# Kernel tuning notes

Hardware: AMD Instinct MI355X
Metric: run time of the kernel (lower is better)

Reference implementation:

```python
import jax, jax.numpy as jnp
import numpy as np

N_NODES = 50000
N_EDGES = 1000000
N_HID = 64
N_GRAPHS = 500
IN_DIM = 4


def setup_inputs() -> dict:
    key = jax.random.key(0)
    ks = jax.random.split(key, 10)
    x = jax.random.normal(ks[0], (N_NODES, IN_DIM), dtype=jnp.float32)
    edge_index = jax.random.randint(ks[1], (2, N_EDGES), 0, N_NODES, dtype=jnp.int64)
    batch = jnp.sort(jax.random.randint(ks[2], (N_NODES,), 0, N_GRAPHS, dtype=jnp.int64))
    # learned parameters (glorot-ish init)
    W1 = jax.random.normal(ks[3], (IN_DIM, N_HID), dtype=jnp.float32) / np.sqrt(IN_DIM)
    b1 = jnp.zeros((N_HID,), dtype=jnp.float32)
    W2 = jax.random.normal(ks[4], (N_HID, N_HID), dtype=jnp.float32) / np.sqrt(N_HID)
    b2 = jnp.zeros((N_HID,), dtype=jnp.float32)
    W3 = jax.random.normal(ks[5], (N_HID, 1), dtype=jnp.float32) / np.sqrt(N_HID)
    b3 = jnp.zeros((1,), dtype=jnp.float32)
    return {"x": x, "edge_index": edge_index, "batch": batch,
            "W1": W1, "b1": b1, "W2": W2, "b2": b2, "W3": W3, "b3": b3}


def gcn_conv(x, W, b, src, dst, num_nodes):
    """PyG GCNConv: x@W, add self-loops, sym deg^-1/2 norm, scatter-add aggregate, +bias."""
    h = x @ W  # [N, D]
    loop = jnp.arange(num_nodes, dtype=src.dtype)
    s = jnp.concatenate([src, loop])  # source nodes (messages gathered from)
    d = jnp.concatenate([dst, loop])  # target nodes (messages scattered to)
    deg = jax.ops.segment_sum(jnp.ones_like(d, dtype=h.dtype), d, num_segments=num_nodes)
    dis = jnp.where(deg > 0, jax.lax.rsqrt(jnp.maximum(deg, 1e-12)), 0.0)
    norm = dis[s] * dis[d]  # [E+N]
    msg = h[s] * norm[:, None]  # gather + scale: the memory-bound hot loop
    out = jax.ops.segment_sum(msg, d, num_segments=num_nodes)
    return out + b


def reference(x, edge_index, batch, W1, b1, W2, b2, W3, b3):
    src, dst = edge_index[0], edge_index[1]
    n = x.shape[0]
    h = gcn_conv(x, W1, b1, src, dst, n)
    h = jax.nn.elu(h)
    # F.dropout with training=False (eval mode) is identity
    h = gcn_conv(h, W2, b2, src, dst, n)
    h = jax.nn.elu(h)
    # scatter-mean pooling over graphs
    sums = jax.ops.segment_sum(h, batch, num_segments=N_GRAPHS)
    cnts = jax.ops.segment_sum(jnp.ones((n,), dtype=h.dtype), batch, num_segments=N_GRAPHS)
    pooled = sums / jnp.maximum(cnts, 1.0)[:, None]
    return pooled @ W3 + b3  # [N_GRAPHS, 1]
```

## Files before the change

kernel.cpp:

```cpp
#include <hip/hip_runtime.h>
#include <hip/hip_fp16.h>
#include <math.h>

#define N_NODES 50000
#define N_EDGES 1000000
#define N_HID 64
#define N_GRAPHS 500
#define IN_DIM 4
#define NPAD 50048

#define BK_SHIFT 7
#define BK_NODES 128
#define NBUCK 391
#define BCAP 3072
#define EPT 16
#define EPW (EPT * 256)
#define NWG_BIN ((N_EDGES + EPW - 1) / EPW)

__global__ void k_init(int* bcur, int* gstart, int* gend, float* sums) {
    int i = blockIdx.x * blockDim.x + threadIdx.x;
    if (i < 512) { bcur[i] = 0; gstart[i] = 0; gend[i] = 0; }
    if (i < N_GRAPHS * N_HID) sums[i] = 0.f;
}

__global__ void k_bin(const int* __restrict__ ei, int* bcur, int* __restrict__ P) {
    __shared__ int hist[NBUCK];
    __shared__ int base[NBUCK];
    int t = threadIdx.x;
    int wg0 = blockIdx.x * EPW;
    for (int b = t; b < NBUCK; b += 256) hist[b] = 0;
    __syncthreads();

    const int4* s4 = (const int4*)ei;
    const int4* d4 = (const int4*)(ei + N_EDGES);
    int rs[EPT], rd[EPT], rl[EPT];
#pragma unroll
    for (int i = 0; i < 4; ++i) {
        int e = wg0 + (i * 256 + t) * 4;
        if (e < N_EDGES) {
            int4 vs = s4[e >> 2];
            int4 vd = d4[e >> 2];
            rs[i * 4 + 0] = vs.x; rd[i * 4 + 0] = vd.x;
            rs[i * 4 + 1] = vs.y; rd[i * 4 + 1] = vd.y;
            rs[i * 4 + 2] = vs.z; rd[i * 4 + 2] = vd.z;
            rs[i * 4 + 3] = vs.w; rd[i * 4 + 3] = vd.w;
            rl[i * 4 + 0] = atomicAdd(&hist[vd.x >> BK_SHIFT], 1);
            rl[i * 4 + 1] = atomicAdd(&hist[vd.y >> BK_SHIFT], 1);
            rl[i * 4 + 2] = atomicAdd(&hist[vd.z >> BK_SHIFT], 1);
            rl[i * 4 + 3] = atomicAdd(&hist[vd.w >> BK_SHIFT], 1);
        } else {
            rd[i * 4 + 0] = rd[i * 4 + 1] = rd[i * 4 + 2] = rd[i * 4 + 3] = -1;
        }
    }
    __syncthreads();
    for (int b = t; b < NBUCK; b += 256) {
        int h = hist[b];
        base[b] = h ? atomicAdd(&bcur[b], h) : 0;
    }
    __syncthreads();
#pragma unroll
    for (int i = 0; i < EPT; ++i) {
        if (rd[i] >= 0) {
            int bk = rd[i] >> BK_SHIFT;
            int loc = base[bk] + rl[i];
            if (loc > BCAP - 1) loc = BCAP - 1;
            P[(size_t)bk * BCAP + loc] = (rs[i] << BK_SHIFT) | (rd[i] & (BK_NODES - 1));
        }
    }
}

__global__ void k_build(const int* __restrict__ bcur, const int* __restrict__ P,
                        const float* __restrict__ x,
                        int* __restrict__ srcidx, int* __restrict__ offs,
                        int* __restrict__ endp, float* __restrict__ dis,
                        float* __restrict__ xs) {
    __shared__ int sp[BCAP];
    __shared__ int scnt[BK_NODES];
    __shared__ int sscan[BK_NODES];
    __shared__ int scur[BK_NODES];
    int b = blockIdx.x;
    int t = threadIdx.x;
    int n = bcur[b];
    if (n > BCAP) n = BCAP;
    if (t < BK_NODES) scnt[t] = 0;
    __syncthreads();
    for (int i = t; i < n; i += 256) {
        int v = P[(size_t)b * BCAP + i];
        sp[i] = v;
        atomicAdd(&scnt[v & (BK_NODES - 1)], 1);
    }
    __syncthreads();
    if (t < BK_NODES) sscan[t] = scnt[t];
    __syncthreads();
    for (int d = 1; d < BK_NODES; d <<= 1) {
        int v = 0;
        if (t < BK_NODES && t >= d) v = sscan[t - d];
        __syncthreads();
        if (t < BK_NODES) sscan[t] += v;
        __syncthreads();
    }
    if (t < BK_NODES) {
        int excl = sscan[t] - scnt[t];
        scur[t] = excl;
        int node = b * BK_NODES + t;
        if (node < N_NODES) {
            int o = b * BCAP + excl;
            offs[node] = o;
            endp[node] = o + scnt[t];
            float dd = 1.0f / sqrtf((float)(scnt[t] + 1));
            dis[node] = dd;
            float4 xv = ((const float4*)x)[node];
            xv.x *= dd; xv.y *= dd; xv.z *= dd; xv.w *= dd;
            ((float4*)xs)[node] = xv;
        }
    }
    __syncthreads();
    for (int i = t; i < n; i += 256) {
        int v = sp[i];
        int ln = v & (BK_NODES - 1);
        int pos = b * BCAP + atomicAdd(&scur[ln], 1);
        srcidx[pos] = v >> BK_SHIFT;
    }
}

__global__ void k_layer1(const float* __restrict__ xs, const int* __restrict__ offs,
                         const int* __restrict__ endp, const int* __restrict__ srcidx,
                         const float* __restrict__ dis, const int* __restrict__ batch,
                         const float* __restrict__ W1, const float* __restrict__ b1,
                         int* __restrict__ gstart, int* __restrict__ gend,
                         __half* __restrict__ h1s) {
    __shared__ float4 sagg[256];
    __shared__ float sdis[256];
    __shared__ float sW1[IN_DIM * N_HID];
    __shared__ float sb1[N_HID];
    int t = threadIdx.x;
    int nb = blockIdx.x * 256;
    int i = nb + t;
    sW1[t] = W1[t];
    if (t < N_HID) sb1[t] = b1[t];
    if (i < N_NODES) {
        int g = batch[i];
        if (i == 0 || batch[i - 1] != g) gstart[g] = i;
        if (i == N_NODES - 1 || batch[i + 1] != g) gend[g] = i + 1;
        const float4* xs4 = (const float4*)xs;
        float4 a0 = xs4[i];
        float4 a1 = make_float4(0.f, 0.f, 0.f, 0.f);
        float4 a2 = a1, a3 = a1;
        int q = offs[i], e = endp[i];
        for (; q + 4 <= e; q += 4) {
            int i0 = srcidx[q], i1 = srcidx[q + 1], i2 = srcidx[q + 2], i3 = srcidx[q + 3];
            float4 v0 = xs4[i0], v1 = xs4[i1], v2 = xs4[i2], v3 = xs4[i3];
            a0.x += v0.x; a0.y += v0.y; a0.z += v0.z; a0.w += v0.w;
            a1.x += v1.x; a1.y += v1.y; a1.z += v1.z; a1.w += v1.w;
            a2.x += v2.x; a2.y += v2.y; a2.z += v2.z; a2.w += v2.w;
            a3.x += v3.x; a3.y += v3.y; a3.z += v3.z; a3.w += v3.w;
        }
        for (; q < e; ++q) {
            float4 v = xs4[srcidx[q]];
            a0.x += v.x; a0.y += v.y; a0.z += v.z; a0.w += v.w;
        }
        float dd = dis[i];
        float4 r;
        r.x = (a0.x + a1.x + a2.x + a3.x) * dd;
        r.y = (a0.y + a1.y + a2.y + a3.y) * dd;
        r.z = (a0.z + a1.z + a2.z + a3.z) * dd;
        r.w = (a0.w + a1.w + a2.w + a3.w) * dd;
        sagg[t] = r;
        sdis[t] = dd;
    } else {
        sagg[t] = make_float4(0.f, 0.f, 0.f, 0.f);
        sdis[t] = 0.f;
    }
    __syncthreads();
    int w = t >> 6, j = t & 63;
    float w0 = sW1[0 * N_HID + j], w1 = sW1[1 * N_HID + j];
    float w2 = sW1[2 * N_HID + j], w3 = sW1[3 * N_HID + j];
    float bj = sb1[j];
    for (int n = 0; n < 64; ++n) {
        int local = w * 64 + n;
        int node = nb + local;
        if (node >= N_NODES) break;
        float4 a = sagg[local];
        float acc = a.x * w0 + a.y * w1 + a.z * w2 + a.w * w3 + bj;
        acc = acc > 0.f ? acc : expm1f(acc);
        h1s[(size_t)node * N_HID + j] = __float2half_rn(acc * sdis[local]);
    }
}

__device__ inline void acc_half8(float* acc, float4 raw) {
    const __half2* hp = (const __half2*)&raw;
#pragma unroll
    for (int c = 0; c < 4; ++c) {
        float2 f = __half22float2(hp[c]);
        acc[2 * c + 0] += f.x;
        acc[2 * c + 1] += f.y;
    }
}

#define L2_NODES 16
__global__ void k_layer2(const __half* __restrict__ h1s, const int* __restrict__ offs,
                         const int* __restrict__ endp, const int* __restrict__ srcidx,
                         const float* __restrict__ dis, const int* __restrict__ batch,
                         const float* __restrict__ W2, const float* __restrict__ b2,
                         float* __restrict__ sums) {
    __shared__ float sAT[N_HID][L2_NODES + 1];
    __shared__ int sbat[L2_NODES];
    int t = threadIdx.x;
    int nb = blockIdx.x * L2_NODES;
    if (t < L2_NODES) sbat[t] = batch[nb + t];

    int wv = t >> 6, lane = t & 63;
    int g = lane >> 3, l = lane & 7;
    const float4* hsv = (const float4*)h1s;
    for (int nn = 0; nn < 4; ++nn) {
        int local = wv * 4 + nn;
        int node = nb + local;
        int start = offs[node], end = endp[node];
        float accA[8] = {0.f, 0.f, 0.f, 0.f, 0.f, 0.f, 0.f, 0.f};
        float accB[8] = {0.f, 0.f, 0.f, 0.f, 0.f, 0.f, 0.f, 0.f};
        if (g == 0) acc_half8(accA, hsv[(size_t)node * 8 + l]);
        for (int base = start; base < end; base += 64) {
            int nc = end - base; if (nc > 64) nc = 64;
            int myidx = (base + lane < end) ? srcidx[base + lane] : 0;
            int q = 0;
            for (; q + 16 <= nc; q += 16) {
                int s0 = __shfl(myidx, q + g);
                int s1 = __shfl(myidx, q + 8 + g);
                float4 r0 = hsv[(size_t)s0 * 8 + l];
                float4 r1 = hsv[(size_t)s1 * 8 + l];
                acc_half8(accA, r0);
                acc_half8(accB, r1);
            }
            if (q + 8 <= nc) {
                int s = __shfl(myidx, q + g);
                acc_half8(accA, hsv[(size_t)s * 8 + l]);
                q += 8;
            }
            {
                int s = __shfl(myidx, q + g);
                if (q + g < nc) acc_half8(accB, hsv[(size_t)s * 8 + l]);
            }
        }
#pragma unroll
        for (int c = 0; c < 8; ++c) accA[c] += accB[c];
#pragma unroll
        for (int c = 0; c < 8; ++c) {
            accA[c] += __shfl_xor(accA[c], 8);
            accA[c] += __shfl_xor(accA[c], 16);
            accA[c] += __shfl_xor(accA[c], 32);
        }
        if (g == 0) {
            float dw = dis[node];
#pragma unroll
            for (int c = 0; c < 8; ++c) sAT[8 * l + c][local] = accA[c] * dw;
        }
    }
    __syncthreads();

    int tj = t & 15, tn = t >> 4;
    const float4* W2v = (const float4*)W2;
    float4 acc = make_float4(0.f, 0.f, 0.f, 0.f);
#pragma unroll 8
    for (int k = 0; k < N_HID; ++k) {
        float a = sAT[k][tn];
        float4 w = W2v[k * 16 + tj];
        acc.x += a * w.x; acc.y += a * w.y; acc.z += a * w.z; acc.w += a * w.w;
    }
    float4 bb = ((const float4*)b2)[tj];
    __syncthreads();
    {
        float4 r;
        r.x = acc.x + bb.x; r.y = acc.y + bb.y;
        r.z = acc.z + bb.z; r.w = acc.w + bb.w;
        r.x = r.x > 0.f ? r.x : expm1f(r.x);
        r.y = r.y > 0.f ? r.y : expm1f(r.y);
        r.z = r.z > 0.f ? r.z : expm1f(r.z);
        r.w = r.w > 0.f ? r.w : expm1f(r.w);
        sAT[4 * tj + 0][tn] = r.x;
        sAT[4 * tj + 1][tn] = r.y;
        sAT[4 * tj + 2][tn] = r.z;
        sAT[4 * tj + 3][tn] = r.w;
    }
    __syncthreads();

    if (t < 64) {
        int s = 0;
        while (s < L2_NODES) {
            int gg = sbat[s];
            int e = s + 1;
            while (e < L2_NODES && sbat[e] == gg) ++e;
            float p = 0.f;
            for (int n = s; n < e; ++n) p += sAT[t][n];
            atomicAdd(&sums[gg * N_HID + t], p);
            s = e;
        }
    }
}

__global__ void k_final(const float* __restrict__ sums, const int* __restrict__ gstart,
                        const int* __restrict__ gend, const float* __restrict__ W3,
                        const float* __restrict__ b3, float* __restrict__ out) {
    int gid = blockIdx.x * 4 + (threadIdx.x >> 6);
    int j = threadIdx.x & 63;
    if (gid >= N_GRAPHS) return;
    int cnt = gend[gid] - gstart[gid];
    float v = sums[gid * N_HID + j] / (float)(cnt > 0 ? cnt : 1);
    float p = v * W3[j];
#pragma unroll
    for (int off = 32; off; off >>= 1) p += __shfl_down(p, off);
    if (j == 0) out[gid] = p + b3[0];
}

extern "C" void kernel_launch(void* const* d_in, const int* in_sizes, int n_in,
                              void* d_out, int out_size, void* d_ws, size_t ws_size,
                              hipStream_t stream) {
    const float* x   = (const float*)d_in[0];
    const int*   ei  = (const int*)d_in[1];
    const int*   bat = (const int*)d_in[2];
    const float* W1  = (const float*)d_in[3];
    const float* b1  = (const float*)d_in[4];
    const float* W2  = (const float*)d_in[5];
    const float* b2  = (const float*)d_in[6];
    const float* W3  = (const float*)d_in[7];
    const float* b3  = (const float*)d_in[8];
    float* out = (float*)d_out;

    char* w = (char*)d_ws;
    int*   bcur   = (int*)w;   w += 512 * 4;
    int*   offs   = (int*)w;   w += NPAD * 4;
    int*   endp   = (int*)w;   w += NPAD * 4;
    float* dis    = (float*)w; w += NPAD * 4;
    int*   gstart = (int*)w;   w += 512 * 4;
    int*   gend   = (int*)w;   w += 512 * 4;
    float* sums   = (float*)w; w += (size_t)N_GRAPHS * N_HID * 4;
    float* xs     = (float*)w; w += (size_t)NPAD * IN_DIM * 4;
    int*   srcidx = (int*)w;   w += (size_t)NBUCK * BCAP * 4;
    int*   P      = (int*)w;   w += (size_t)NBUCK * BCAP * 4;
    __half* h1s   = (__half*)w; w += (size_t)N_NODES * N_HID * 2;

    const int B = 256;
    const int gN = (N_NODES + B - 1) / B;

    k_init<<<(N_GRAPHS * N_HID + B - 1) / B, B, 0, stream>>>(bcur, gstart, gend, sums);
    k_bin<<<NWG_BIN, B, 0, stream>>>(ei, bcur, P);
    k_build<<<NBUCK, B, 0, stream>>>(bcur, P, x, srcidx, offs, endp, dis, xs);

    k_layer1<<<gN, B, 0, stream>>>(xs, offs, endp, srcidx, dis, bat, W1, b1,
                                   gstart, gend, h1s);

    k_layer2<<<N_NODES / L2_NODES, B, 0, stream>>>(
        h1s, offs, endp, srcidx, dis, bat, W2, b2, sums);

    k_final<<<(N_GRAPHS + 3) / 4, B, 0, stream>>>(sums, gstart, gend, W3, b3, out);
}
```

Baseline: 99.60 us.

## Split layer-1 features into two half planes and gather each in separate passes

Layer 1 now writes its fp16 output as two 32-column planes instead of one 64-column row per node. Layer 2 makes two passes, each gathering only one plane, so the working set each pass touches is half the size and fits the cache better. It also prefetches the next node's offsets and source indices before reducing the current node. The cost is that the edge index lists are read twice, each gather moves 8 bytes instead of 16, and the number of gather instructions doubles.

```diff
diff --git a/kernel.cpp b/kernel.cpp
--- a/kernel.cpp
+++ b/kernel.cpp
@@ -128,7 +128,7 @@
                          const float* __restrict__ dis, const int* __restrict__ batch,
                          const float* __restrict__ W1, const float* __restrict__ b1,
                          int* __restrict__ gstart, int* __restrict__ gend,
-                         __half* __restrict__ h1s) {
+                         __half* __restrict__ h1a, __half* __restrict__ h1b) {
     __shared__ float4 sagg[256];
     __shared__ float sdis[256];
     __shared__ float sW1[IN_DIM * N_HID];
@@ -183,26 +183,25 @@
         float4 a = sagg[local];
         float acc = a.x * w0 + a.y * w1 + a.z * w2 + a.w * w3 + bj;
         acc = acc > 0.f ? acc : expm1f(acc);
-        h1s[(size_t)node * N_HID + j] = __float2half_rn(acc * sdis[local]);
-    }
-}
-
-__device__ inline void acc_half8(float* acc, float4 raw) {
+        __half hv = __float2half_rn(acc * sdis[local]);
+        if (j < 32) h1a[(size_t)node * 32 + j] = hv;
+        else        h1b[(size_t)node * 32 + (j - 32)] = hv;
+    }
+}
+
+__device__ inline void acc_half4(float* acc, float2 raw) {
     const __half2* hp = (const __half2*)&raw;
-#pragma unroll
-    for (int c = 0; c < 4; ++c) {
-        float2 f = __half22float2(hp[c]);
-        acc[2 * c + 0] += f.x;
-        acc[2 * c + 1] += f.y;
-    }
+    float2 f0 = __half22float2(hp[0]);
+    float2 f1 = __half22float2(hp[1]);
+    acc[0] += f0.x; acc[1] += f0.y; acc[2] += f1.x; acc[3] += f1.y;
 }
 
 #define L2_NODES 16
-__global__ void k_layer2(const __half* __restrict__ h1s, const int* __restrict__ offs,
-                         const int* __restrict__ endp, const int* __restrict__ srcidx,
-                         const float* __restrict__ dis, const int* __restrict__ batch,
-                         const float* __restrict__ W2, const float* __restrict__ b2,
-                         float* __restrict__ sums) {
+__global__ void k_layer2(const __half* __restrict__ h1a, const __half* __restrict__ h1b,
+                         const int* __restrict__ offs, const int* __restrict__ endp,
+                         const int* __restrict__ srcidx, const float* __restrict__ dis,
+                         const int* __restrict__ batch, const float* __restrict__ W2,
+                         const float* __restrict__ b2, float* __restrict__ sums) {
     __shared__ float sAT[N_HID][L2_NODES + 1];
     __shared__ int sbat[L2_NODES];
     int t = threadIdx.x;
@@ -211,48 +210,63 @@
 
     int wv = t >> 6, lane = t & 63;
     int g = lane >> 3, l = lane & 7;
-    const float4* hsv = (const float4*)h1s;
-    for (int nn = 0; nn < 4; ++nn) {
-        int local = wv * 4 + nn;
-        int node = nb + local;
+#pragma unroll
+    for (int p = 0; p < 2; ++p) {
+        const float2* hv = (const float2*)(p == 0 ? h1a : h1b);
+        int node = nb + wv * 4;
         int start = offs[node], end = endp[node];
-        float accA[8] = {0.f, 0.f, 0.f, 0.f, 0.f, 0.f, 0.f, 0.f};
-        float accB[8] = {0.f, 0.f, 0.f, 0.f, 0.f, 0.f, 0.f, 0.f};
-        if (g == 0) acc_half8(accA, hsv[(size_t)node * 8 + l]);
-        for (int base = start; base < end; base += 64) {
-            int nc = end - base; if (nc > 64) nc = 64;
-            int myidx = (base + lane < end) ? srcidx[base + lane] : 0;
-            int q = 0;
-            for (; q + 16 <= nc; q += 16) {
-                int s0 = __shfl(myidx, q + g);
-                int s1 = __shfl(myidx, q + 8 + g);
-                float4 r0 = hsv[(size_t)s0 * 8 + l];
-                float4 r1 = hsv[(size_t)s1 * 8 + l];
-                acc_half8(accA, r0);
-                acc_half8(accB, r1);
+        int myidx = (start + lane < end) ? srcidx[start + lane] : 0;
+        for (int nn = 0; nn < 4; ++nn) {
+            float accA[4] = {0.f, 0.f, 0.f, 0.f};
+            float accB[4] = {0.f, 0.f, 0.f, 0.f};
+            if (g == 0) acc_half4(accA, hv[(size_t)node * 8 + l]);
+            int base = start;
+            for (;;) {
+                int nc = end - base; if (nc > 64) nc = 64;
+                int q = 0;
+                for (; q + 16 <= nc; q += 16) {
+                    int s0 = __shfl(myidx, q + g);
+                    int s1 = __shfl(myidx, q + 8 + g);
+                    float2 r0 = hv[(size_t)s0 * 8 + l];
+                    float2 r1 = hv[(size_t)s1 * 8 + l];
+                    acc_half4(accA, r0);
+                    acc_half4(accB, r1);
+                }
+                if (q + 8 <= nc) {
+                    int s = __shfl(myidx, q + g);
+                    acc_half4(accA, hv[(size_t)s * 8 + l]);
+                    q += 8;
+                }
+                if (q < nc) {
+                    int s = __shfl(myidx, q + g);
+                    if (q + g < nc) acc_half4(accB, hv[(size_t)s * 8 + l]);
+                }
+                base += 64;
+                if (base >= end) break;
+                myidx = (base + lane < end) ? srcidx[base + lane] : 0;
             }
-            if (q + 8 <= nc) {
-                int s = __shfl(myidx, q + g);
-                acc_half8(accA, hsv[(size_t)s * 8 + l]);
-                q += 8;
+            int node_n = 0, start_n = 0, end_n = 0, myidx_n = 0;
+            if (nn < 3) {
+                node_n = nb + wv * 4 + nn + 1;
+                start_n = offs[node_n]; end_n = endp[node_n];
+                myidx_n = (start_n + lane < end_n) ? srcidx[start_n + lane] : 0;
             }
-            {
-                int s = __shfl(myidx, q + g);
-                if (q + g < nc) acc_half8(accB, hsv[(size_t)s * 8 + l]);
+#pragma unroll
+            for (int c = 0; c < 4; ++c) accA[c] += accB[c];
+#pragma unroll
+            for (int c = 0; c < 4; ++c) {
+                accA[c] += __shfl_xor(accA[c], 8);
+                accA[c] += __shfl_xor(accA[c], 16);
+                accA[c] += __shfl_xor(accA[c], 32);
             }
-        }
-#pragma unroll
-        for (int c = 0; c < 8; ++c) accA[c] += accB[c];
-#pragma unroll
-        for (int c = 0; c < 8; ++c) {
-            accA[c] += __shfl_xor(accA[c], 8);
-            accA[c] += __shfl_xor(accA[c], 16);
-            accA[c] += __shfl_xor(accA[c], 32);
-        }
-        if (g == 0) {
-            float dw = dis[node];
-#pragma unroll
-            for (int c = 0; c < 8; ++c) sAT[8 * l + c][local] = accA[c] * dw;
+            if (g == 0) {
+                int local = wv * 4 + nn;
+                float dw = dis[node];
+#pragma unroll
+                for (int c = 0; c < 4; ++c)
+                    sAT[p * 32 + 4 * l + c][local] = accA[c] * dw;
+            }
+            node = node_n; start = start_n; end = end_n; myidx = myidx_n;
         }
     }
     __syncthreads();
@@ -336,7 +350,8 @@
     float* xs     = (float*)w; w += (size_t)NPAD * IN_DIM * 4;
     int*   srcidx = (int*)w;   w += (size_t)NBUCK * BCAP * 4;
     int*   P      = (int*)w;   w += (size_t)NBUCK * BCAP * 4;
-    __half* h1s   = (__half*)w; w += (size_t)N_NODES * N_HID * 2;
+    __half* h1a   = (__half*)w; w += (size_t)NPAD * 32 * 2;
+    __half* h1b   = (__half*)w; w += (size_t)NPAD * 32 * 2;
 
     const int B = 256;
     const int gN = (N_NODES + B - 1) / B;
@@ -346,10 +361,10 @@
     k_build<<<NBUCK, B, 0, stream>>>(bcur, P, x, srcidx, offs, endp, dis, xs);
 
     k_layer1<<<gN, B, 0, stream>>>(xs, offs, endp, srcidx, dis, bat, W1, b1,
-                                   gstart, gend, h1s);
+                                   gstart, gend, h1a, h1b);
 
     k_layer2<<<N_NODES / L2_NODES, B, 0, stream>>>(
-        h1s, offs, endp, srcidx, dis, bat, W2, b2, sums);
+        h1a, h1b, offs, endp, srcidx, dis, bat, W2, b2, sums);
 
     k_final<<<(N_GRAPHS + 3) / 4, B, 0, stream>>>(sums, gstart, gend, W3, b3, out);
 }
```

Measured after the change: 116.3 us. 16.8% more time.

## Interleave neighbor gathers for four nodes per wave in layer-2 aggregation

Applied to the files above, without the earlier changes.

The layer-2 aggregation now processes its four nodes per wave together instead of one after another. Each iteration issues up to eight independent 16-byte gathers (two per node) before accumulating, which raises memory-level parallelism and hides the load latency of the irregular gathers. A launch-bounds hint of four blocks of 256 threads is added to hold occupancy. The cost is more registers for the four accumulator sets and per-node predication, and waves with skewed degrees keep looping for the longest node.

```diff
diff --git a/kernel.cpp b/kernel.cpp
--- a/kernel.cpp
+++ b/kernel.cpp
@@ -198,11 +198,12 @@
 }
 
 #define L2_NODES 16
-__global__ void k_layer2(const __half* __restrict__ h1s, const int* __restrict__ offs,
-                         const int* __restrict__ endp, const int* __restrict__ srcidx,
-                         const float* __restrict__ dis, const int* __restrict__ batch,
-                         const float* __restrict__ W2, const float* __restrict__ b2,
-                         float* __restrict__ sums) {
+__global__ void __launch_bounds__(256, 4)
+k_layer2(const __half* __restrict__ h1s, const int* __restrict__ offs,
+         const int* __restrict__ endp, const int* __restrict__ srcidx,
+         const float* __restrict__ dis, const int* __restrict__ batch,
+         const float* __restrict__ W2, const float* __restrict__ b2,
+         float* __restrict__ sums) {
     __shared__ float sAT[N_HID][L2_NODES + 1];
     __shared__ int sbat[L2_NODES];
     int t = threadIdx.x;
@@ -212,66 +213,101 @@
     int wv = t >> 6, lane = t & 63;
     int g = lane >> 3, l = lane & 7;
     const float4* hsv = (const float4*)h1s;
+    int nodeA = nb + wv * 4;
+
+    int en[4], win[4], q[4], nc[4], idx[4];
+    float acc[4][8];
+#pragma unroll
     for (int nn = 0; nn < 4; ++nn) {
-        int local = wv * 4 + nn;
-        int node = nb + local;
-        int start = offs[node], end = endp[node];
-        float accA[8] = {0.f, 0.f, 0.f, 0.f, 0.f, 0.f, 0.f, 0.f};
-        float accB[8] = {0.f, 0.f, 0.f, 0.f, 0.f, 0.f, 0.f, 0.f};
-        if (g == 0) acc_half8(accA, hsv[(size_t)node * 8 + l]);
-        for (int base = start; base < end; base += 64) {
-            int nc = end - base; if (nc > 64) nc = 64;
-            int myidx = (base + lane < end) ? srcidx[base + lane] : 0;
-            int q = 0;
-            for (; q + 16 <= nc; q += 16) {
-                int s0 = __shfl(myidx, q + g);
-                int s1 = __shfl(myidx, q + 8 + g);
-                float4 r0 = hsv[(size_t)s0 * 8 + l];
-                float4 r1 = hsv[(size_t)s1 * 8 + l];
-                acc_half8(accA, r0);
-                acc_half8(accB, r1);
+        int node = nodeA + nn;
+        int s = offs[node];
+        en[nn] = endp[node];
+        win[nn] = s;
+        int rem = en[nn] - s;
+        nc[nn] = rem > 64 ? 64 : rem;
+        q[nn] = 0;
+        idx[nn] = (s + lane < en[nn]) ? srcidx[s + lane] : 0;
+#pragma unroll
+        for (int c = 0; c < 8; ++c) acc[nn][c] = 0.f;
+    }
+    if (g == 0) {
+#pragma unroll
+        for (int nn = 0; nn < 4; ++nn)
+            acc_half8(acc[nn], hsv[(size_t)(nodeA + nn) * 8 + l]);
+    }
+
+    bool any = (nc[0] > 0) | (nc[1] > 0) | (nc[2] > 0) | (nc[3] > 0);
+    while (any) {
+        any = false;
+        float4 r0[4], r1[4];
+        bool p0[4], p1[4], act[4];
+#pragma unroll
+        for (int nn = 0; nn < 4; ++nn) {
+            act[nn] = q[nn] < nc[nn];
+            p0[nn] = p1[nn] = false;
+            if (act[nn]) {
+                int s0 = __shfl(idx[nn], q[nn] + g);
+                int s1 = __shfl(idx[nn], q[nn] + 8 + g);
+                p0[nn] = q[nn] + g < nc[nn];
+                p1[nn] = q[nn] + 8 + g < nc[nn];
+                if (p0[nn]) r0[nn] = hsv[(size_t)s0 * 8 + l];
+                if (p1[nn]) r1[nn] = hsv[(size_t)s1 * 8 + l];
             }
-            if (q + 8 <= nc) {
-                int s = __shfl(myidx, q + g);
-                acc_half8(accA, hsv[(size_t)s * 8 + l]);
-                q += 8;
+        }
+#pragma unroll
+        for (int nn = 0; nn < 4; ++nn) {
+            if (act[nn]) {
+                if (p0[nn]) acc_half8(acc[nn], r0[nn]);
+                if (p1[nn]) acc_half8(acc[nn], r1[nn]);
+                q[nn] += 16;
+                if (q[nn] >= nc[nn] && win[nn] + 64 < en[nn]) {
+                    win[nn] += 64;
+                    int rem = en[nn] - win[nn];
+                    nc[nn] = rem > 64 ? 64 : rem;
+                    q[nn] = 0;
+                    idx[nn] = (win[nn] + lane < en[nn]) ? srcidx[win[nn] + lane] : 0;
+                }
+                if (q[nn] < nc[nn]) any = true;
             }
-            {
-                int s = __shfl(myidx, q + g);
-                if (q + g < nc) acc_half8(accB, hsv[(size_t)s * 8 + l]);
-            }
-        }
-#pragma unroll
-        for (int c = 0; c < 8; ++c) accA[c] += accB[c];
+        }
+    }
+#pragma unroll
+    for (int nn = 0; nn < 4; ++nn) {
 #pragma unroll
         for (int c = 0; c < 8; ++c) {
-            accA[c] += __shfl_xor(accA[c], 8);
-            accA[c] += __shfl_xor(accA[c], 16);
-            accA[c] += __shfl_xor(accA[c], 32);
-        }
-        if (g == 0) {
-            float dw = dis[node];
-#pragma unroll
-            for (int c = 0; c < 8; ++c) sAT[8 * l + c][local] = accA[c] * dw;
+            float v = acc[nn][c];
+            v += __shfl_xor(v, 8);
+            v += __shfl_xor(v, 16);
+            v += __shfl_xor(v, 32);
+            acc[nn][c] = v;
+        }
+    }
+    if (g == 0) {
+#pragma unroll
+        for (int nn = 0; nn < 4; ++nn) {
+            float dw = dis[nodeA + nn];
+            int local = wv * 4 + nn;
+#pragma unroll
+            for (int c = 0; c < 8; ++c) sAT[8 * l + c][local] = acc[nn][c] * dw;
         }
     }
     __syncthreads();
 
     int tj = t & 15, tn = t >> 4;
     const float4* W2v = (const float4*)W2;
-    float4 acc = make_float4(0.f, 0.f, 0.f, 0.f);
+    float4 gacc = make_float4(0.f, 0.f, 0.f, 0.f);
 #pragma unroll 8
     for (int k = 0; k < N_HID; ++k) {
         float a = sAT[k][tn];
         float4 w = W2v[k * 16 + tj];
-        acc.x += a * w.x; acc.y += a * w.y; acc.z += a * w.z; acc.w += a * w.w;
+        gacc.x += a * w.x; gacc.y += a * w.y; gacc.z += a * w.z; gacc.w += a * w.w;
     }
     float4 bb = ((const float4*)b2)[tj];
     __syncthreads();
     {
         float4 r;
-        r.x = acc.x + bb.x; r.y = acc.y + bb.y;
-        r.z = acc.z + bb.z; r.w = acc.w + bb.w;
+        r.x = gacc.x + bb.x; r.y = gacc.y + bb.y;
+        r.z = gacc.z + bb.z; r.w = gacc.w + bb.w;
         r.x = r.x > 0.f ? r.x : expm1f(r.x);
         r.y = r.y > 0.f ? r.y : expm1f(r.y);
         r.z = r.z > 0.f ? r.z : expm1f(r.z);
```

Result: slower. 106.1 us (+6.5%).

## Split layer-2 into per-node aggregation kernel and separate GEMM+pool kernel

Applied to the files above, without the earlier changes.

The fused layer-2 kernel, where each wave aggregated four nodes serially, is replaced by two kernels. The first aggregates one node per wave across the whole grid and writes fp32 results to a new global buffer. The second loads 64 nodes per block, runs the W2 GEMM with a 4x4 register tile per thread, applies ELU and pools into the per-graph sums. This aims for more parallelism in the gather and better GEMM reuse, at the cost of an extra 12.8MB fp32 round trip and one more launch.

```diff
diff --git a/kernel.cpp b/kernel.cpp
--- a/kernel.cpp
+++ b/kernel.cpp
@@ -197,103 +197,125 @@
     }
 }
 
-#define L2_NODES 16
-__global__ void k_layer2(const __half* __restrict__ h1s, const int* __restrict__ offs,
-                         const int* __restrict__ endp, const int* __restrict__ srcidx,
-                         const float* __restrict__ dis, const int* __restrict__ batch,
-                         const float* __restrict__ W2, const float* __restrict__ b2,
-                         float* __restrict__ sums) {
-    __shared__ float sAT[N_HID][L2_NODES + 1];
-    __shared__ int sbat[L2_NODES];
+__global__ void k_agg16(const __half* __restrict__ h1s, const int* __restrict__ offs,
+                        const int* __restrict__ endp, const int* __restrict__ srcidx,
+                        const float* __restrict__ dis, float* __restrict__ tmp2) {
+    int wid = (blockIdx.x * blockDim.x + threadIdx.x) >> 6;
+    int lane = threadIdx.x & 63;
+    int g = lane >> 3, l = lane & 7;
+    if (wid >= N_NODES) return;
+    const float4* hsv = (const float4*)h1s;
+    float accA[8] = {0.f, 0.f, 0.f, 0.f, 0.f, 0.f, 0.f, 0.f};
+    float accB[8] = {0.f, 0.f, 0.f, 0.f, 0.f, 0.f, 0.f, 0.f};
+    if (g == 0) acc_half8(accA, hsv[(size_t)wid * 8 + l]);
+    int start = offs[wid], end = endp[wid];
+    for (int base = start; base < end; base += 64) {
+        int nc = end - base; if (nc > 64) nc = 64;
+        int myidx = (base + lane < end) ? srcidx[base + lane] : 0;
+        int q = 0;
+        for (; q + 16 <= nc; q += 16) {
+            int s0 = __shfl(myidx, q + g);
+            int s1 = __shfl(myidx, q + 8 + g);
+            float4 r0 = hsv[(size_t)s0 * 8 + l];
+            float4 r1 = hsv[(size_t)s1 * 8 + l];
+            acc_half8(accA, r0);
+            acc_half8(accB, r1);
+        }
+        if (q + 8 <= nc) {
+            int s = __shfl(myidx, q + g);
+            acc_half8(accA, hsv[(size_t)s * 8 + l]);
+            q += 8;
+        }
+        {
+            int s = __shfl(myidx, q + g);
+            if (q + g < nc) acc_half8(accB, hsv[(size_t)s * 8 + l]);
+        }
+    }
+#pragma unroll
+    for (int c = 0; c < 8; ++c) accA[c] += accB[c];
+#pragma unroll
+    for (int c = 0; c < 8; ++c) {
+        accA[c] += __shfl_xor(accA[c], 8);
+        accA[c] += __shfl_xor(accA[c], 16);
+        accA[c] += __shfl_xor(accA[c], 32);
+    }
+    if (g == 0) {
+        float dw = dis[wid];
+        float4 v0 = make_float4(accA[0] * dw, accA[1] * dw, accA[2] * dw, accA[3] * dw);
+        float4 v1 = make_float4(accA[4] * dw, accA[5] * dw, accA[6] * dw, accA[7] * dw);
+        ((float4*)tmp2)[(size_t)wid * 16 + 2 * l] = v0;
+        ((float4*)tmp2)[(size_t)wid * 16 + 2 * l + 1] = v1;
+    }
+}
+
+#define GP_NODES 64
+__global__ void k_gemmpool(const float* __restrict__ tmp2, const int* __restrict__ batch,
+                           const float* __restrict__ W2, const float* __restrict__ b2,
+                           float* __restrict__ sums) {
+    __shared__ float sAT[N_HID][68];
+    __shared__ int sbat[GP_NODES];
     int t = threadIdx.x;
-    int nb = blockIdx.x * L2_NODES;
-    if (t < L2_NODES) sbat[t] = batch[nb + t];
-
-    int wv = t >> 6, lane = t & 63;
-    int g = lane >> 3, l = lane & 7;
-    const float4* hsv = (const float4*)h1s;
-    for (int nn = 0; nn < 4; ++nn) {
-        int local = wv * 4 + nn;
-        int node = nb + local;
-        int start = offs[node], end = endp[node];
-        float accA[8] = {0.f, 0.f, 0.f, 0.f, 0.f, 0.f, 0.f, 0.f};
-        float accB[8] = {0.f, 0.f, 0.f, 0.f, 0.f, 0.f, 0.f, 0.f};
-        if (g == 0) acc_half8(accA, hsv[(size_t)node * 8 + l]);
-        for (int base = start; base < end; base += 64) {
-            int nc = end - base; if (nc > 64) nc = 64;
-            int myidx = (base + lane < end) ? srcidx[base + lane] : 0;
-            int q = 0;
-            for (; q + 16 <= nc; q += 16) {
-                int s0 = __shfl(myidx, q + g);
-                int s1 = __shfl(myidx, q + 8 + g);
-                float4 r0 = hsv[(size_t)s0 * 8 + l];
-                float4 r1 = hsv[(size_t)s1 * 8 + l];
-                acc_half8(accA, r0);
-                acc_half8(accB, r1);
-            }
-            if (q + 8 <= nc) {
-                int s = __shfl(myidx, q + g);
-                acc_half8(accA, hsv[(size_t)s * 8 + l]);
-                q += 8;
-            }
-            {
-                int s = __shfl(myidx, q + g);
-                if (q + g < nc) acc_half8(accB, hsv[(size_t)s * 8 + l]);
-            }
-        }
-#pragma unroll
-        for (int c = 0; c < 8; ++c) accA[c] += accB[c];
-#pragma unroll
-        for (int c = 0; c < 8; ++c) {
-            accA[c] += __shfl_xor(accA[c], 8);
-            accA[c] += __shfl_xor(accA[c], 16);
-            accA[c] += __shfl_xor(accA[c], 32);
-        }
-        if (g == 0) {
-            float dw = dis[node];
-#pragma unroll
-            for (int c = 0; c < 8; ++c) sAT[8 * l + c][local] = accA[c] * dw;
-        }
-    }
-    __syncthreads();
-
+    int nb = blockIdx.x * GP_NODES;
+    if (t < GP_NODES) sbat[t] = (nb + t < N_NODES) ? batch[nb + t] : -1;
+    {
+        int sn = t >> 2, k0 = (t & 3) * 16;
+        int node = nb + sn;
+        bool ok = node < N_NODES;
+        const float4* a4 = (const float4*)&tmp2[(size_t)(ok ? node : 0) * N_HID];
+#pragma unroll
+        for (int i = 0; i < 4; ++i) {
+            float4 v = ok ? a4[k0 / 4 + i] : make_float4(0.f, 0.f, 0.f, 0.f);
+            sAT[k0 + 4 * i + 0][sn] = v.x;
+            sAT[k0 + 4 * i + 1][sn] = v.y;
+            sAT[k0 + 4 * i + 2][sn] = v.z;
+            sAT[k0 + 4 * i + 3][sn] = v.w;
+        }
+    }
+    __syncthreads();
     int tj = t & 15, tn = t >> 4;
     const float4* W2v = (const float4*)W2;
-    float4 acc = make_float4(0.f, 0.f, 0.f, 0.f);
+    float4 acc0 = make_float4(0.f, 0.f, 0.f, 0.f);
+    float4 acc1 = acc0, acc2 = acc0, acc3 = acc0;
 #pragma unroll 8
     for (int k = 0; k < N_HID; ++k) {
-        float a = sAT[k][tn];
+        float4 a = *(const float4*)&sAT[k][4 * tn];
         float4 w = W2v[k * 16 + tj];
-        acc.x += a * w.x; acc.y += a * w.y; acc.z += a * w.z; acc.w += a * w.w;
+        acc0.x += a.x * w.x; acc0.y += a.x * w.y; acc0.z += a.x * w.z; acc0.w += a.x * w.w;
+        acc1.x += a.y * w.x; acc1.y += a.y * w.y; acc1.z += a.y * w.z; acc1.w += a.y * w.w;
+        acc2.x += a.z * w.x; acc2.y += a.z * w.y; acc2.z += a.z * w.z; acc2.w += a.z * w.w;
+        acc3.x += a.w * w.x; acc3.y += a.w * w.y; acc3.z += a.w * w.z; acc3.w += a.w * w.w;
     }
     float4 bb = ((const float4*)b2)[tj];
     __syncthreads();
-    {
-        float4 r;
-        r.x = acc.x + bb.x; r.y = acc.y + bb.y;
-        r.z = acc.z + bb.z; r.w = acc.w + bb.w;
-        r.x = r.x > 0.f ? r.x : expm1f(r.x);
-        r.y = r.y > 0.f ? r.y : expm1f(r.y);
-        r.z = r.z > 0.f ? r.z : expm1f(r.z);
-        r.w = r.w > 0.f ? r.w : expm1f(r.w);
-        sAT[4 * tj + 0][tn] = r.x;
-        sAT[4 * tj + 1][tn] = r.y;
-        sAT[4 * tj + 2][tn] = r.z;
-        sAT[4 * tj + 3][tn] = r.w;
-    }
-    __syncthreads();
-
-    if (t < 64) {
-        int s = 0;
-        while (s < L2_NODES) {
-            int gg = sbat[s];
-            int e = s + 1;
-            while (e < L2_NODES && sbat[e] == gg) ++e;
+#define GP_WB(ACC, I)                                                         \
+    {                                                                         \
+        float4 r;                                                             \
+        r.x = ACC.x + bb.x; r.y = ACC.y + bb.y;                               \
+        r.z = ACC.z + bb.z; r.w = ACC.w + bb.w;                               \
+        r.x = r.x > 0.f ? r.x : expm1f(r.x);                                  \
+        r.y = r.y > 0.f ? r.y : expm1f(r.y);                                  \
+        r.z = r.z > 0.f ? r.z : expm1f(r.z);                                  \
+        r.w = r.w > 0.f ? r.w : expm1f(r.w);                                  \
+        sAT[4 * tj + 0][4 * tn + (I)] = r.x;                                  \
+        sAT[4 * tj + 1][4 * tn + (I)] = r.y;                                  \
+        sAT[4 * tj + 2][4 * tn + (I)] = r.z;                                  \
+        sAT[4 * tj + 3][4 * tn + (I)] = r.w;                                  \
+    }
+    GP_WB(acc0, 0) GP_WB(acc1, 1) GP_WB(acc2, 2) GP_WB(acc3, 3)
+#undef GP_WB
+    __syncthreads();
+    int j = t & 63, w = t >> 6;
+    int s = 0;
+    while (s < GP_NODES) {
+        int gg = sbat[s];
+        int e = s + 1;
+        while (e < GP_NODES && sbat[e] == gg) ++e;
+        if (gg >= 0 && s + w < e) {
             float p = 0.f;
-            for (int n = s; n < e; ++n) p += sAT[t][n];
-            atomicAdd(&sums[gg * N_HID + t], p);
-            s = e;
-        }
+            for (int n = s + w; n < e; n += 4) p += sAT[j][n];
+            atomicAdd(&sums[gg * N_HID + j], p);
+        }
+        s = e;
     }
 }
 
@@ -337,9 +359,11 @@
     int*   srcidx = (int*)w;   w += (size_t)NBUCK * BCAP * 4;
     int*   P      = (int*)w;   w += (size_t)NBUCK * BCAP * 4;
     __half* h1s   = (__half*)w; w += (size_t)N_NODES * N_HID * 2;
+    float* tmp2   = (float*)w; w += (size_t)N_NODES * N_HID * 4;
 
     const int B = 256;
     const int gN = (N_NODES + B - 1) / B;
+    const int gW = (N_NODES * 64 + B - 1) / B;
 
     k_init<<<(N_GRAPHS * N_HID + B - 1) / B, B, 0, stream>>>(bcur, gstart, gend, sums);
     k_bin<<<NWG_BIN, B, 0, stream>>>(ei, bcur, P);
@@ -348,8 +372,9 @@
     k_layer1<<<gN, B, 0, stream>>>(xs, offs, endp, srcidx, dis, bat, W1, b1,
                                    gstart, gend, h1s);
 
-    k_layer2<<<N_NODES / L2_NODES, B, 0, stream>>>(
-        h1s, offs, endp, srcidx, dis, bat, W2, b2, sums);
+    k_agg16<<<gW, B, 0, stream>>>(h1s, offs, endp, srcidx, dis, tmp2);
+    k_gemmpool<<<(N_NODES + GP_NODES - 1) / GP_NODES, B, 0, stream>>>(
+        tmp2, bat, W2, b2, sums);
 
     k_final<<<(N_GRAPHS + 3) / 4, B, 0, stream>>>(sums, gstart, gend, W3, b3, out);
 }
```

New measurement: 97.01 us. -2.6%, faster.
